# Optimization experiments

Measured on AMD Instinct MI355X. Metric: run time of the kernel, lower is better.

The kernel has to match this reference:

```python
import jax, jax.numpy as jnp
import numpy as np

B, S, E, H = 4, 2048, 1024, 16
D = E // H  # head_dim = 64


def setup_inputs() -> dict:
    key = jax.random.key(0)
    ks = jax.random.split(key, 6)
    x = jax.random.normal(ks[0], (B, S, E), dtype=jnp.float32)
    # realistic padding: per-batch valid lengths in [S//2, S]
    lengths = jax.random.randint(ks[1], (B,), S // 2, S + 1)
    padding_mask = jnp.arange(S)[None, :] < lengths[:, None]  # [B,S] bool
    init = 1.0 / np.sqrt(E)
    qkv_w = jax.random.uniform(ks[2], (3 * E, E), jnp.float32, -init, init)
    qkv_b = jnp.zeros((3 * E,), jnp.float32)
    proj_w = jax.random.uniform(ks[3], (E, E), jnp.float32, -init, init)
    proj_b = jnp.zeros((E,), jnp.float32)
    return {"x": x, "padding_mask": padding_mask, "qkv_w": qkv_w,
            "qkv_b": qkv_b, "proj_w": proj_w, "proj_b": proj_b}


def reference(x, padding_mask, qkv_w, qkv_b, proj_w, proj_b):
    b, s, e = x.shape
    scale = D ** -0.5
    qkv = x @ qkv_w.T + qkv_b                      # [B,S,3E]
    qkv = qkv.reshape(b, s, 3, H, D).transpose(2, 0, 3, 1, 4)  # [3,B,H,S,D]
    q, k, v = qkv[0], qkv[1], qkv[2]
    attn = jnp.einsum('bhsd,bhtd->bhst', q, k) * scale         # [B,H,S,S]
    attn = jnp.where(padding_mask[:, None, None, :], attn, -jnp.inf)
    attn = jax.nn.softmax(attn, axis=-1)
    out = jnp.einsum('bhst,bhtd->bhsd', attn, v)               # [B,H,S,D]
    out = out.transpose(0, 2, 1, 3).reshape(b, s, e)           # [B,S,E]
    return out @ proj_w.T + proj_b
```

## Files before the change

### kernel.cpp

```cpp
#include <hip/hip_runtime.h>
#include <hip/hip_bf16.h>
#include <stdint.h>

#define S_LEN 2048
#define NB 4
#define NH 16
#define HD 64
#define E_DIM 1024

typedef __attribute__((ext_vector_type(8))) short s16x8;
typedef __attribute__((ext_vector_type(4))) float f32x4;
typedef __attribute__((ext_vector_type(16))) float f32x16;
typedef __attribute__((ext_vector_type(4))) int i32x4;
typedef __attribute__((ext_vector_type(2))) unsigned u32x2;

__device__ __forceinline__ short f2bf(float f) {
  union { float f; uint32_t u; } x; x.f = f;
  uint32_t r = (x.u + 0x7FFF + ((x.u >> 16) & 1)) >> 16;
  return (short)r;
}

__device__ __forceinline__ int cvtpk_bf16(float lo, float hi) {
  int r;
  asm("v_cvt_pk_bf16_f32 %0, %1, %2" : "=v"(r) : "v"(lo), "v"(hi));
  return r;
}

__device__ __forceinline__ u32x2 pl32(unsigned a, unsigned b) {
  auto r = __builtin_amdgcn_permlane32_swap(a, b, false, false);
  return (u32x2){(unsigned)r[0], (unsigned)r[1]};
}
__device__ __forceinline__ float pl32_max(float v) {
  unsigned u = __builtin_bit_cast(unsigned, v);
  u32x2 r = pl32(u, u);
  return fmaxf(__builtin_bit_cast(float, r[0]), __builtin_bit_cast(float, r[1]));
}
__device__ __forceinline__ float pl32_sum(float v) {
  unsigned u = __builtin_bit_cast(unsigned, v);
  u32x2 r = pl32(u, u);
  return __builtin_bit_cast(float, r[0]) + __builtin_bit_cast(float, r[1]);
}

__device__ __forceinline__ void glds16(const void* g, void* l) {
  __builtin_amdgcn_global_load_lds(
      (const __attribute__((address_space(1))) unsigned int*)g,
      (__attribute__((address_space(3))) unsigned int*)l, 16, 0, 0);
}

__global__ void cvt_f32_bf16(const float* __restrict__ src, short* __restrict__ dst, int n4) {
  int i = blockIdx.x * blockDim.x + threadIdx.x;
  if (i < n4) {
    float4 v = reinterpret_cast<const float4*>(src)[i];
    short4 o;
    o.x = f2bf(v.x); o.y = f2bf(v.y); o.z = f2bf(v.z); o.w = f2bf(v.w);
    reinterpret_cast<short4*>(dst)[i] = o;
  }
}

__global__ void compute_lengths(const unsigned char* __restrict__ mask, int* __restrict__ lengths) {
  int b = blockIdx.x;
  unsigned char b0 = mask[0], b1 = mask[1];
  int mode = (b0 == 0) ? 2 : ((b1 != 0) ? 0 : 1);
  int cnt = 0;
  for (int s = threadIdx.x; s < S_LEN; s += blockDim.x) {
    bool v;
    if (mode == 0)      v = mask[(size_t)b * S_LEN + s] != 0;
    else if (mode == 1) v = reinterpret_cast<const int*>(mask)[(size_t)b * S_LEN + s] != 0;
    else                v = reinterpret_cast<const float*>(mask)[(size_t)b * S_LEN + s] != 0.f;
    cnt += v ? 1 : 0;
  }
  __shared__ int red[256];
  red[threadIdx.x] = cnt;
  __syncthreads();
  for (int o = 128; o > 0; o >>= 1) {
    if (threadIdx.x < o) red[threadIdx.x] += red[threadIdx.x + o];
    __syncthreads();
  }
  if (threadIdx.x == 0) lengths[b] = red[0];
}

template <int MODE>
__launch_bounds__(256, 3)
__global__ void gemm_nt(const short* __restrict__ A, const short* __restrict__ Bw,
                        const float* __restrict__ bias, float* __restrict__ Cout,
                        short* __restrict__ Qo, short* __restrict__ Ko, short* __restrict__ Vo,
                        int M, int N, int K) {
  __shared__ short Al[2][128 * 32];
  __shared__ short Bl[2][128 * 32];
  const int tid = threadIdx.x;
  const int lane = tid & 63;
  const int w = tid >> 6;
  const int wm = w >> 1, wn = w & 1;
  const int l15 = lane & 15, l4 = lane >> 4;
  const int flat = blockIdx.y * gridDim.x + blockIdx.x;
  const int cpx = (gridDim.x * gridDim.y) >> 3;
  const int nf = (flat & 7) * cpx + (flat >> 3);
  const int bm = nf & 63;
  const int bn = nf >> 6;

  const int srow = w * 32 + (lane >> 2);
  const int scol = (lane & 3) * 8;
  const short* Ag = A + (size_t)(bm * 128 + srow) * K + scol;
  const short* Bg = Bw + (size_t)(bn * 128 + srow) * K + scol;
  const size_t row16 = (size_t)16 * K;

  f32x4 acc[4][4];
#pragma unroll
  for (int i = 0; i < 4; ++i)
#pragma unroll
    for (int j = 0; j < 4; ++j) acc[i][j] = (f32x4){0.f, 0.f, 0.f, 0.f};

  auto stage = [&](int kt, int buf) {
    const short* a0 = Ag + kt * 32;
    const short* b0 = Bg + kt * 32;
    short* Asm = &Al[buf][(w * 32) * 32];
    short* Bsm = &Bl[buf][(w * 32) * 32];
    glds16(a0, Asm);
    glds16(a0 + row16, Asm + 16 * 32);
    glds16(b0, Bsm);
    glds16(b0 + row16, Bsm + 16 * 32);
  };

  const int NT = K / 32;
  stage(0, 0);
  __syncthreads();
  for (int kt = 0; kt < NT; ++kt) {
    const int cur = kt & 1;
    if (kt + 1 < NT) stage(kt + 1, cur ^ 1);
    s16x8 af[4], bf[4];
#pragma unroll
    for (int mi = 0; mi < 4; ++mi)
      af[mi] = *reinterpret_cast<const s16x8*>(&Al[cur][(wm * 64 + mi * 16 + l15) * 32 + l4 * 8]);
#pragma unroll
    for (int nj = 0; nj < 4; ++nj)
      bf[nj] = *reinterpret_cast<const s16x8*>(&Bl[cur][(wn * 64 + nj * 16 + l15) * 32 + l4 * 8]);
#pragma unroll
    for (int mi = 0; mi < 4; ++mi)
#pragma unroll
      for (int nj = 0; nj < 4; ++nj)
        acc[mi][nj] = __builtin_amdgcn_mfma_f32_16x16x32_bf16(af[mi], bf[nj], acc[mi][nj], 0, 0, 0);
    __syncthreads();
  }

#pragma unroll
  for (int mi = 0; mi < 4; ++mi) {
#pragma unroll
    for (int nj = 0; nj < 4; ++nj) {
      const int m0 = bm * 128 + wm * 64 + mi * 16 + l4 * 4;
      const int n = bn * 128 + wn * 64 + nj * 16 + l15;
      const float bv = bias[n];
      if (MODE == 0) {
#pragma unroll
        for (int r = 0; r < 4; ++r)
          Cout[(size_t)(m0 + r) * N + n] = acc[mi][nj][r] + bv;
      } else {
        const int which = n >> 10, e = n & 1023, h = e >> 6, d = e & 63;
        const int b = m0 >> 11, s = m0 & 2047;
        const size_t bh = (size_t)(b * NH + h);
        if (which == 2) {
          short4 pk;
          pk.x = f2bf(acc[mi][nj][0] + bv); pk.y = f2bf(acc[mi][nj][1] + bv);
          pk.z = f2bf(acc[mi][nj][2] + bv); pk.w = f2bf(acc[mi][nj][3] + bv);
          *reinterpret_cast<short4*>(&Vo[(bh * HD + d) * S_LEN + s]) = pk;
        } else if (which == 0) {
#pragma unroll
          for (int r = 0; r < 4; ++r)
            Qo[(bh * S_LEN + s + r) * HD + d] = f2bf((acc[mi][nj][r] + bv) * 0.180336880111f);
        } else {
#pragma unroll
          for (int r = 0; r < 4; ++r)
            Ko[(bh * S_LEN + s + r) * HD + d] = f2bf(acc[mi][nj][r] + bv);
        }
      }
    }
  }
}

__launch_bounds__(256, 3)
__global__ void attn_fwd(const short* __restrict__ Q, const short* __restrict__ K,
                         const short* __restrict__ Vt, short* __restrict__ ctx,
                         const int* __restrict__ lengths) {
  __shared__ short Kl[2][64 * 64];
  __shared__ short Vl[2][64 * 64];
  const int tid = threadIdx.x;
  const int lane = tid & 63, w = tid >> 6;
  const int l31 = lane & 31, hi = lane >> 5;
  const int bid = blockIdx.x;
  const int xcd = bid & 7, idx = bid >> 3;
  const int sub = idx & 7, qt = idx >> 3;
  const int bh = sub * 8 + xcd;
  const int b = bh >> 4;
  const int len = lengths[b];

  const size_t bhS = (size_t)bh * S_LEN;
  const int qrow = qt * 128 + w * 32 + l31;
  const short* Qb = Q + (bhS + qrow) * HD + hi * 8;
  s16x8 qf0 = *reinterpret_cast<const s16x8*>(Qb);
  s16x8 qf1 = *reinterpret_cast<const s16x8*>(Qb + 16);
  s16x8 qf2 = *reinterpret_cast<const s16x8*>(Qb + 32);
  s16x8 qf3 = *reinterpret_cast<const s16x8*>(Qb + 48);

  const int rr = lane >> 3, bb = lane & 7;
  const int swz = (bb ^ rr) << 4;
  const char* KgB = (const char*)(K + bhS * HD);
  const char* VgB = (const char*)(Vt + bhS * HD);
  const int krow0 = 16 * w + rr;
  const size_t koff0 = (size_t)krow0 * 128 + swz;
  const size_t koff1 = (size_t)(krow0 + 8) * 128 + swz;
  const size_t voff0 = (size_t)krow0 * (S_LEN * 2) + swz;
  const size_t voff1 = (size_t)(krow0 + 8) * (S_LEN * 2) + swz;

  auto stage = [&](int kt, int buf) {
    const char* ks = KgB + (size_t)kt * (64 * 128);
    const char* vs = VgB + (size_t)kt * 128;
    short* kd = &Kl[buf][w * 1024];
    short* vd = &Vl[buf][w * 1024];
    glds16(ks + koff0, kd);
    glds16(ks + koff1, kd + 512);
    glds16(vs + voff0, vd);
    glds16(vs + voff1, vd + 512);
  };

  f32x16 o0, o1;
#pragma unroll
  for (int r = 0; r < 16; ++r) { o0[r] = 0.f; o1[r] = 0.f; }
  float m_run = -3e38f, l_run = 0.f;

  const int sw = (l31 & 7) << 4;

  auto tile_body = [&](int kt, int buf) {
    const char* kb = (const char*)&Kl[buf][0];
    const char* vb = (const char*)&Vl[buf][0];
    f32x16 sa0, sa1;
#pragma unroll
    for (int r = 0; r < 16; ++r) { sa0[r] = 0.f; sa1[r] = 0.f; }
    __builtin_amdgcn_s_setprio(1);
#pragma unroll
    for (int n = 0; n < 4; ++n) {
      s16x8 kf = *reinterpret_cast<const s16x8*>(kb + l31 * 128 + ((n * 32 + hi * 16) ^ sw));
      const s16x8 q = (n == 0) ? qf0 : (n == 1) ? qf1 : (n == 2) ? qf2 : qf3;
      sa0 = __builtin_amdgcn_mfma_f32_32x32x16_bf16(kf, q, sa0, 0, 0, 0);
    }
#pragma unroll
    for (int n = 0; n < 4; ++n) {
      s16x8 kf = *reinterpret_cast<const s16x8*>(kb + (32 + l31) * 128 + ((n * 32 + hi * 16) ^ sw));
      const s16x8 q = (n == 0) ? qf0 : (n == 1) ? qf1 : (n == 2) ? qf2 : qf3;
      sa1 = __builtin_amdgcn_mfma_f32_32x32x16_bf16(kf, q, sa1, 0, 0, 0);
    }
    __builtin_amdgcn_s_setprio(0);
    const int mrem = len - kt * 64;
    if (mrem < 64) {
#pragma unroll
      for (int r = 0; r < 16; ++r) {
        int off = (r & 3) + 8 * (r >> 2) + 4 * hi;
        if (off >= mrem) sa0[r] = -3e38f;
        if (off + 32 >= mrem) sa1[r] = -3e38f;
      }
    }
    float a0 = fmaxf(fmaxf(sa0[0], sa0[1]), sa0[2]);
    float a1 = fmaxf(fmaxf(sa0[3], sa0[4]), sa0[5]);
    float a2 = fmaxf(fmaxf(sa0[6], sa0[7]), sa0[8]);
    float a3 = fmaxf(fmaxf(sa0[9], sa0[10]), sa0[11]);
    float a4 = fmaxf(fmaxf(sa0[12], sa0[13]), sa0[14]);
    float a5 = fmaxf(fmaxf(sa0[15], sa1[0]), sa1[1]);
    float a6 = fmaxf(fmaxf(sa1[2], sa1[3]), sa1[4]);
    float a7 = fmaxf(fmaxf(sa1[5], sa1[6]), sa1[7]);
    float a8 = fmaxf(fmaxf(sa1[8], sa1[9]), sa1[10]);
    float a9 = fmaxf(fmaxf(sa1[11], sa1[12]), sa1[13]);
    float aa = fmaxf(sa1[14], sa1[15]);
    a0 = fmaxf(fmaxf(a0, a1), a2);
    a3 = fmaxf(fmaxf(a3, a4), a5);
    a6 = fmaxf(fmaxf(a6, a7), a8);
    a9 = fmaxf(a9, aa);
    float mx = pl32_max(fmaxf(fmaxf(a0, a3), fmaxf(a6, a9)));
    if (!__all(mx <= m_run + 8.f)) {
      float mnew = fmaxf(m_run, mx);
      float al = exp2f(m_run - mnew);
#pragma unroll
      for (int r = 0; r < 16; ++r) { o0[r] *= al; o1[r] *= al; }
      l_run *= al;
      m_run = mnew;
    }
    float s0 = 0.f, s1 = 0.f;
#pragma unroll
    for (int r = 0; r < 16; ++r) {
      sa0[r] = exp2f(sa0[r] - m_run);
      sa1[r] = exp2f(sa1[r] - m_run);
      s0 += sa0[r];
      s1 += sa1[r];
    }
    l_run += pl32_sum(s0 + s1);
    union { i32x4 i; s16x8 h; } uf[4];
#pragma unroll
    for (int sb = 0; sb < 2; ++sb) {
      const f32x16& sa = sb ? sa1 : sa0;
      unsigned A0 = cvtpk_bf16(sa[0], sa[1]),   B0 = cvtpk_bf16(sa[2], sa[3]);
      unsigned A1 = cvtpk_bf16(sa[4], sa[5]),   B1 = cvtpk_bf16(sa[6], sa[7]);
      unsigned A2 = cvtpk_bf16(sa[8], sa[9]),   B2 = cvtpk_bf16(sa[10], sa[11]);
      unsigned A3 = cvtpk_bf16(sa[12], sa[13]), B3 = cvtpk_bf16(sa[14], sa[15]);
      u32x2 rA01 = pl32(A0, A1);
      u32x2 rB01 = pl32(B0, B1);
      u32x2 rA23 = pl32(A2, A3);
      u32x2 rB23 = pl32(B2, B3);
      uf[sb * 2 + 0].i = (i32x4){(int)rA01[0], (int)rB01[0], (int)rA01[1], (int)rB01[1]};
      uf[sb * 2 + 1].i = (i32x4){(int)rA23[0], (int)rB23[0], (int)rA23[1], (int)rB23[1]};
    }
    __builtin_amdgcn_s_setprio(1);
#pragma unroll
    for (int kc = 0; kc < 4; ++kc) {
      s16x8 v0 = *reinterpret_cast<const s16x8*>(vb + l31 * 128 + ((kc * 32 + hi * 16) ^ sw));
      o0 = __builtin_amdgcn_mfma_f32_32x32x16_bf16(v0, uf[kc].h, o0, 0, 0, 0);
    }
#pragma unroll
    for (int kc = 0; kc < 4; ++kc) {
      s16x8 v1 = *reinterpret_cast<const s16x8*>(vb + (32 + l31) * 128 + ((kc * 32 + hi * 16) ^ sw));
      o1 = __builtin_amdgcn_mfma_f32_32x32x16_bf16(v1, uf[kc].h, o1, 0, 0, 0);
    }
    __builtin_amdgcn_s_setprio(0);
  };

  const int ntt = (len + 63) >> 6;
  stage(0, 0);
  __syncthreads();
  for (int kt = 0; kt < ntt; ++kt) {
    const int buf = kt & 1;
    if (kt + 1 < ntt) stage(kt + 1, buf ^ 1);
    tile_body(kt, buf);
    __syncthreads();
  }

  const float inv = 1.f / l_run;
  const int h = bh & 15;
  const size_t base = ((size_t)b * S_LEN + qrow) * E_DIM + h * HD + 4 * hi;
#pragma unroll
  for (int rq = 0; rq < 4; ++rq) {
    short4 a, c;
    a.x = f2bf(o0[4 * rq + 0] * inv); a.y = f2bf(o0[4 * rq + 1] * inv);
    a.z = f2bf(o0[4 * rq + 2] * inv); a.w = f2bf(o0[4 * rq + 3] * inv);
    *reinterpret_cast<short4*>(&ctx[base + 8 * rq]) = a;
    c.x = f2bf(o1[4 * rq + 0] * inv); c.y = f2bf(o1[4 * rq + 1] * inv);
    c.z = f2bf(o1[4 * rq + 2] * inv); c.w = f2bf(o1[4 * rq + 3] * inv);
    *reinterpret_cast<short4*>(&ctx[base + 32 + 8 * rq]) = c;
  }
}

extern "C" void kernel_launch(void* const* d_in, const int* in_sizes, int n_in,
                              void* d_out, int out_size, void* d_ws, size_t ws_size,
                              hipStream_t stream) {
  const float* x = (const float*)d_in[0];
  const unsigned char* mask = (const unsigned char*)d_in[1];
  const float* qkv_w = (const float*)d_in[2];
  const float* qkv_b = (const float*)d_in[3];
  const float* proj_w = (const float*)d_in[4];
  const float* proj_b = (const float*)d_in[5];
  float* out = (float*)d_out;

  const size_t SZ_X = (size_t)NB * S_LEN * E_DIM;
  short* xb = (short*)d_ws;
  short* wqb = xb + SZ_X;
  short* wpb = wqb + (size_t)3 * E_DIM * E_DIM;
  short* Qs = wpb + (size_t)E_DIM * E_DIM;
  short* Ks = Qs + SZ_X;
  short* Vts = Ks + SZ_X;
  short* ctx = Vts + SZ_X;
  int* lens = (int*)(ctx + SZ_X);

  cvt_f32_bf16<<<(int)(SZ_X / 4 / 256), 256, 0, stream>>>(x, xb, (int)(SZ_X / 4));
  cvt_f32_bf16<<<3 * E_DIM * E_DIM / 4 / 256, 256, 0, stream>>>(qkv_w, wqb, 3 * E_DIM * E_DIM / 4);
  cvt_f32_bf16<<<E_DIM * E_DIM / 4 / 256, 256, 0, stream>>>(proj_w, wpb, E_DIM * E_DIM / 4);
  compute_lengths<<<NB, 256, 0, stream>>>(mask, lens);

  dim3 g1(3 * E_DIM / 128, NB * S_LEN / 128);
  gemm_nt<1><<<g1, 256, 0, stream>>>(xb, wqb, qkv_b, nullptr, Qs, Ks, Vts,
                                     NB * S_LEN, 3 * E_DIM, E_DIM);

  attn_fwd<<<NB * NH * (S_LEN / 128), 256, 0, stream>>>(Qs, Ks, Vts, ctx, lens);

  dim3 g2(E_DIM / 128, NB * S_LEN / 128);
  gemm_nt<0><<<g2, 256, 0, stream>>>(ctx, wpb, proj_b, out, nullptr, nullptr, nullptr,
                                     NB * S_LEN, E_DIM, E_DIM);
}
```

Baseline: 332.0 us.

## Restructure attention LDS layout to column-chunk order and compute row sums via MFMA

Staging of K and V into LDS changes from a row-major XOR-swizzled layout to a layout grouped by 16-byte column chunk, so each lane reads contiguous 16-byte slices without swizzle arithmetic. The two separate MFMA loops for the upper and lower 32-key halves are interleaved so their K/V loads and MFMAs alternate. The softmax denominator is no longer summed with VALU adds and a permlane reduction. It is accumulated by an extra MFMA against a ones vector, which moves that work onto the matrix unit but adds four MFMAs per tile and another 16-register accumulator that could reduce occupancy.

```diff
diff --git a/kernel.cpp b/kernel.cpp
--- a/kernel.cpp
+++ b/kernel.cpp
@@ -34,11 +34,6 @@
   unsigned u = __builtin_bit_cast(unsigned, v);
   u32x2 r = pl32(u, u);
   return fmaxf(__builtin_bit_cast(float, r[0]), __builtin_bit_cast(float, r[1]));
-}
-__device__ __forceinline__ float pl32_sum(float v) {
-  unsigned u = __builtin_bit_cast(unsigned, v);
-  u32x2 r = pl32(u, u);
-  return __builtin_bit_cast(float, r[0]) + __builtin_bit_cast(float, r[1]);
 }
 
 __device__ __forceinline__ void glds16(const void* g, void* l) {
@@ -180,8 +175,8 @@
 __global__ void attn_fwd(const short* __restrict__ Q, const short* __restrict__ K,
                          const short* __restrict__ Vt, short* __restrict__ ctx,
                          const int* __restrict__ lengths) {
-  __shared__ short Kl[2][64 * 64];
-  __shared__ short Vl[2][64 * 64];
+  __shared__ short Kl[2][8 * 512];
+  __shared__ short Vl[2][8 * 512];
   const int tid = threadIdx.x;
   const int lane = tid & 63, w = tid >> 6;
   const int l31 = lane & 31, hi = lane >> 5;
@@ -200,52 +195,44 @@
   s16x8 qf2 = *reinterpret_cast<const s16x8*>(Qb + 32);
   s16x8 qf3 = *reinterpret_cast<const s16x8*>(Qb + 48);
 
-  const int rr = lane >> 3, bb = lane & 7;
-  const int swz = (bb ^ rr) << 4;
-  const char* KgB = (const char*)(K + bhS * HD);
-  const char* VgB = (const char*)(Vt + bhS * HD);
-  const int krow0 = 16 * w + rr;
-  const size_t koff0 = (size_t)krow0 * 128 + swz;
-  const size_t koff1 = (size_t)(krow0 + 8) * 128 + swz;
-  const size_t voff0 = (size_t)krow0 * (S_LEN * 2) + swz;
-  const size_t voff1 = (size_t)(krow0 + 8) * (S_LEN * 2) + swz;
+  const char* KgL = (const char*)(K + bhS * HD) + (size_t)lane * 128;
+  const char* VgL = (const char*)(Vt + bhS * HD) + (size_t)lane * (S_LEN * 2);
 
   auto stage = [&](int kt, int buf) {
-    const char* ks = KgB + (size_t)kt * (64 * 128);
-    const char* vs = VgB + (size_t)kt * 128;
-    short* kd = &Kl[buf][w * 1024];
-    short* vd = &Vl[buf][w * 1024];
-    glds16(ks + koff0, kd);
-    glds16(ks + koff1, kd + 512);
-    glds16(vs + voff0, vd);
-    glds16(vs + voff1, vd + 512);
+    const char* ks = KgL + (size_t)kt * 8192;
+    const char* vs = VgL + (size_t)kt * 128;
+    const int g0 = 2 * w, g1 = 2 * w + 1;
+    glds16(ks + g0 * 16, &Kl[buf][g0 * 512]);
+    glds16(ks + g1 * 16, &Kl[buf][g1 * 512]);
+    glds16(vs + g0 * 16, &Vl[buf][g0 * 512]);
+    glds16(vs + g1 * 16, &Vl[buf][g1 * 512]);
   };
 
-  f32x16 o0, o1;
-#pragma unroll
-  for (int r = 0; r < 16; ++r) { o0[r] = 0.f; o1[r] = 0.f; }
-  float m_run = -3e38f, l_run = 0.f;
-
-  const int sw = (l31 & 7) << 4;
+  f32x16 o0, o1, acc_l;
+#pragma unroll
+  for (int r = 0; r < 16; ++r) { o0[r] = 0.f; o1[r] = 0.f; acc_l[r] = 0.f; }
+  float m_run = -3e38f;
+
+  s16x8 aone;
+#pragma unroll
+  for (int j = 0; j < 8; ++j) aone[j] = (short)0x3F80;
+
+  const int ro = l31 * 16;
 
   auto tile_body = [&](int kt, int buf) {
-    const char* kb = (const char*)&Kl[buf][0];
-    const char* vb = (const char*)&Vl[buf][0];
+    const char* kbh = (const char*)&Kl[buf][0] + hi * 1024;
+    const char* vbh = (const char*)&Vl[buf][0] + hi * 1024;
     f32x16 sa0, sa1;
 #pragma unroll
     for (int r = 0; r < 16; ++r) { sa0[r] = 0.f; sa1[r] = 0.f; }
     __builtin_amdgcn_s_setprio(1);
 #pragma unroll
     for (int n = 0; n < 4; ++n) {
-      s16x8 kf = *reinterpret_cast<const s16x8*>(kb + l31 * 128 + ((n * 32 + hi * 16) ^ sw));
+      s16x8 kf0 = *reinterpret_cast<const s16x8*>(kbh + n * 2048 + ro);
+      s16x8 kf1 = *reinterpret_cast<const s16x8*>(kbh + n * 2048 + 512 + ro);
       const s16x8 q = (n == 0) ? qf0 : (n == 1) ? qf1 : (n == 2) ? qf2 : qf3;
-      sa0 = __builtin_amdgcn_mfma_f32_32x32x16_bf16(kf, q, sa0, 0, 0, 0);
-    }
-#pragma unroll
-    for (int n = 0; n < 4; ++n) {
-      s16x8 kf = *reinterpret_cast<const s16x8*>(kb + (32 + l31) * 128 + ((n * 32 + hi * 16) ^ sw));
-      const s16x8 q = (n == 0) ? qf0 : (n == 1) ? qf1 : (n == 2) ? qf2 : qf3;
-      sa1 = __builtin_amdgcn_mfma_f32_32x32x16_bf16(kf, q, sa1, 0, 0, 0);
+      sa0 = __builtin_amdgcn_mfma_f32_32x32x16_bf16(kf0, q, sa0, 0, 0, 0);
+      sa1 = __builtin_amdgcn_mfma_f32_32x32x16_bf16(kf1, q, sa1, 0, 0, 0);
     }
     __builtin_amdgcn_s_setprio(0);
     const int mrem = len - kt * 64;
@@ -278,18 +265,14 @@
       float al = exp2f(m_run - mnew);
 #pragma unroll
       for (int r = 0; r < 16; ++r) { o0[r] *= al; o1[r] *= al; }
-      l_run *= al;
+      acc_l[0] *= al;
       m_run = mnew;
     }
-    float s0 = 0.f, s1 = 0.f;
 #pragma unroll
     for (int r = 0; r < 16; ++r) {
       sa0[r] = exp2f(sa0[r] - m_run);
       sa1[r] = exp2f(sa1[r] - m_run);
-      s0 += sa0[r];
-      s1 += sa1[r];
-    }
-    l_run += pl32_sum(s0 + s1);
+    }
     union { i32x4 i; s16x8 h; } uf[4];
 #pragma unroll
     for (int sb = 0; sb < 2; ++sb) {
@@ -308,13 +291,11 @@
     __builtin_amdgcn_s_setprio(1);
 #pragma unroll
     for (int kc = 0; kc < 4; ++kc) {
-      s16x8 v0 = *reinterpret_cast<const s16x8*>(vb + l31 * 128 + ((kc * 32 + hi * 16) ^ sw));
+      s16x8 v0 = *reinterpret_cast<const s16x8*>(vbh + kc * 2048 + ro);
+      s16x8 v1 = *reinterpret_cast<const s16x8*>(vbh + kc * 2048 + 512 + ro);
       o0 = __builtin_amdgcn_mfma_f32_32x32x16_bf16(v0, uf[kc].h, o0, 0, 0, 0);
-    }
-#pragma unroll
-    for (int kc = 0; kc < 4; ++kc) {
-      s16x8 v1 = *reinterpret_cast<const s16x8*>(vb + (32 + l31) * 128 + ((kc * 32 + hi * 16) ^ sw));
       o1 = __builtin_amdgcn_mfma_f32_32x32x16_bf16(v1, uf[kc].h, o1, 0, 0, 0);
+      acc_l = __builtin_amdgcn_mfma_f32_32x32x16_bf16(aone, uf[kc].h, acc_l, 0, 0, 0);
     }
     __builtin_amdgcn_s_setprio(0);
   };
@@ -329,7 +310,7 @@
     __syncthreads();
   }
 
-  const float inv = 1.f / l_run;
+  const float inv = 1.f / acc_l[0];
   const int h = bh & 15;
   const size_t base = ((size_t)b * S_LEN + qrow) * E_DIM + h * HD + 4 * hi;
 #pragma unroll
```

Result: slower. 340.3 us (+2.5%).
